# Optimization experiments

Hardware: AMD Instinct MI355X
Metric: run time of the kernel (lower is better)

Reference implementation:

```python
import jax, jax.numpy as jnp
import numpy as np

NEG_SLOPE = 0.2
EPS = 1e-16
HEADS1, OUT1 = 4, 32
HEADS2, OUT2 = 1, 32


def _gat_conv(x, W, a_src, a_dst, bias, src, dst, num_nodes, heads, out_c, concat):
    # x: [N, F_in], W: [F_in, heads*out_c], a_*: [heads, out_c]
    h = (x @ W).reshape(num_nodes, heads, out_c)            # [N, H, C]
    alpha_src = (h * a_src).sum(-1)                          # [N, H]
    alpha_dst = (h * a_dst).sum(-1)                          # [N, H]
    e = jax.nn.leaky_relu(alpha_src[src] + alpha_dst[dst], NEG_SLOPE)  # [E, H]
    # softmax over incoming edges of each destination node (PyG softmax)
    m = jax.ops.segment_max(e, dst, num_segments=num_nodes)
    ex = jnp.exp(e - m[dst])
    s = jax.ops.segment_sum(ex, dst, num_segments=num_nodes)
    alpha = ex / (s[dst] + EPS)                              # [E, H]
    out = jax.ops.segment_sum(h[src] * alpha[:, :, None], dst,
                              num_segments=num_nodes)        # [N, H, C]
    out = out.reshape(num_nodes, heads * out_c) if concat else out.mean(axis=1)
    return out + bias


def setup_inputs() -> dict:
    key = jax.random.key(0)
    ks = jax.random.split(key, 10)
    N, E, F_IN = 50000, 1600000, 128
    sc = 0.1
    return {
        "x": jax.random.normal(ks[0], (N, F_IN), jnp.float32),
        "edge_index": jax.random.randint(ks[1], (2, E), 0, N, jnp.int32),
        "W1": jax.random.normal(ks[2], (F_IN, HEADS1 * OUT1), jnp.float32) * sc,
        "a_src1": jax.random.normal(ks[3], (HEADS1, OUT1), jnp.float32) * sc,
        "a_dst1": jax.random.normal(ks[4], (HEADS1, OUT1), jnp.float32) * sc,
        "b1": jax.random.normal(ks[5], (HEADS1 * OUT1,), jnp.float32) * sc,
        "W2": jax.random.normal(ks[6], (HEADS1 * OUT1, HEADS2 * OUT2), jnp.float32) * sc,
        "a_src2": jax.random.normal(ks[7], (HEADS2, OUT2), jnp.float32) * sc,
        "a_dst2": jax.random.normal(ks[8], (HEADS2, OUT2), jnp.float32) * sc,
        "b2": jax.random.normal(ks[9], (OUT2,), jnp.float32) * sc,
    }


def reference(x, edge_index, W1, a_src1, a_dst1, b1, W2, a_src2, a_dst2, b2):
    N = x.shape[0]
    # PyG GATConv default add_self_loops=True
    loops = jnp.arange(N, dtype=edge_index.dtype)
    src = jnp.concatenate([edge_index[0], loops])
    dst = jnp.concatenate([edge_index[1], loops])
    h = _gat_conv(x, W1, a_src1, a_dst1, b1, src, dst, N, HEADS1, OUT1, True)
    h = jax.nn.elu(h)
    return _gat_conv(h, W2, a_src2, a_dst2, b2, src, dst, N, HEADS2, OUT2, False)
```

## Files before the change

### kernel.cpp

```cpp
#include <hip/hip_runtime.h>
#include <math.h>

#define NEG_SLOPE 0.2f
#define EPSV 1e-16f
#define NPART 16

typedef _Float16 half4 __attribute__((ext_vector_type(4)));
typedef _Float16 half8 __attribute__((ext_vector_type(8)));


__global__ void k_hist_rank(const int* __restrict__ ei, int E, int ET, int N,
                            int* __restrict__ degp, int* __restrict__ rank){
    int i = blockIdx.x * 256 + threadIdx.x;
    if (i < ET){
        int d = (i < E) ? ei[E + i] : (i - E);
        int p = blockIdx.x & (NPART - 1);
        rank[i] = atomicAdd(&degp[p * N + d], 1);
    }
}

__global__ void k_scan_blk(const int* __restrict__ degp, int N,
                           int* __restrict__ rowptr, int* __restrict__ bsum){
    int b = blockIdx.x, t = threadIdx.x;
    int base = b * 1024 + t * 4;
    int v[4];
    #pragma unroll
    for (int j = 0; j < 4; j++){
        int n = base + j, s = 0;
        if (n < N){
            #pragma unroll
            for (int p = 0; p < NPART; p++) s += degp[p * N + n];
        }
        v[j] = s;
    }
    int s = v[0] + v[1] + v[2] + v[3];
    int lane = t & 63, wid = t >> 6;
    int x = s;
    #pragma unroll
    for (int off = 1; off < 64; off <<= 1){
        int y = __shfl_up(x, off, 64);
        if (lane >= off) x += y;
    }
    __shared__ int ws[4];
    if (lane == 63) ws[wid] = x;
    __syncthreads();
    int woff = 0;
    for (int w = 0; w < wid; w++) woff += ws[w];
    int run = woff + x - s;
    #pragma unroll
    for (int j = 0; j < 4; j++){
        if (base + j < N) rowptr[base + j] = run;
        run += v[j];
    }
    if (t == 255) bsum[b] = woff + x;
}

__global__ void k_finalize(const int* __restrict__ bsum, const int* __restrict__ degp,
                           int N, int ET,
                           int* __restrict__ rowptr, int* __restrict__ poff){
    int b = blockIdx.x, t = threadIdx.x;
    int n = b * 256 + t;
    int chunk = (b * 256) >> 10;
    int off = 0;
    for (int c = 0; c < chunk; c++) off += bsum[c];
    if (n < N){
        int r = rowptr[n] + off;
        rowptr[n] = r;
        int run = r;
        #pragma unroll
        for (int p = 0; p < NPART; p++){
            poff[p * N + n] = run;
            run += degp[p * N + n];
        }
    }
    if (n == 0) rowptr[N] = ET;
}

__launch_bounds__(256)
__global__ void k_scatter2(const int* __restrict__ ei, int E, int ET, int N,
                           const int* __restrict__ poff, const int* __restrict__ rank,
                           int* __restrict__ csr_src){
    int i = blockIdx.x * 256 + threadIdx.x;
    if (i >= ET) return;
    int s, d;
    if (i < E){ s = ei[i]; d = ei[E + i]; } else { s = i - E; d = s; }
    int p = blockIdx.x & (NPART - 1);
    csr_src[poff[p * N + d] + rank[i]] = s;
}


__launch_bounds__(256)
__global__ void k_gemm1(const float* __restrict__ x, const float* __restrict__ W1,
                        const float* __restrict__ a_src, const float* __restrict__ a_dst,
                        _Float16* __restrict__ h1h, float* __restrict__ asrc1,
                        float* __restrict__ adst1, int N){
    __shared__ float Wl[128 * 128];
    __shared__ float xl[32 * 128];
    int t = threadIdx.x;
    int cg = t & 31, ns = t >> 5;
    for (int idx = t; idx < 4096; idx += 256)
        *(float4*)&Wl[idx * 4] = *(const float4*)&W1[idx * 4];
    int n0 = blockIdx.x * 32;
    for (int idx = t; idx < 1024; idx += 256){
        int row = idx >> 5, k4 = idx & 31;
        float4 v = {0.f, 0.f, 0.f, 0.f};
        if (n0 + row < N) v = *(const float4*)&x[(size_t)(n0 + row) * 128 + k4 * 4];
        *(float4*)&xl[row * 128 + k4 * 4] = v;
    }
    __syncthreads();
    float4 acc0 = {0,0,0,0}, acc1 = {0,0,0,0}, acc2 = {0,0,0,0}, acc3 = {0,0,0,0};
    #pragma unroll 2
    for (int k = 0; k < 128; k += 4){
        float4 xv0 = *(float4*)&xl[(ns     ) * 128 + k];
        float4 xv1 = *(float4*)&xl[(ns +  8) * 128 + k];
        float4 xv2 = *(float4*)&xl[(ns + 16) * 128 + k];
        float4 xv3 = *(float4*)&xl[(ns + 24) * 128 + k];
        #pragma unroll
        for (int kk = 0; kk < 4; kk++){
            float4 w = *(float4*)&Wl[(k + kk) * 128 + cg * 4];
            float x0 = ((float*)&xv0)[kk];
            float x1 = ((float*)&xv1)[kk];
            float x2v= ((float*)&xv2)[kk];
            float x3 = ((float*)&xv3)[kk];
            acc0.x = fmaf(x0, w.x, acc0.x); acc0.y = fmaf(x0, w.y, acc0.y);
            acc0.z = fmaf(x0, w.z, acc0.z); acc0.w = fmaf(x0, w.w, acc0.w);
            acc1.x = fmaf(x1, w.x, acc1.x); acc1.y = fmaf(x1, w.y, acc1.y);
            acc1.z = fmaf(x1, w.z, acc1.z); acc1.w = fmaf(x1, w.w, acc1.w);
            acc2.x = fmaf(x2v, w.x, acc2.x); acc2.y = fmaf(x2v, w.y, acc2.y);
            acc2.z = fmaf(x2v, w.z, acc2.z); acc2.w = fmaf(x2v, w.w, acc2.w);
            acc3.x = fmaf(x3, w.x, acc3.x); acc3.y = fmaf(x3, w.y, acc3.y);
            acc3.z = fmaf(x3, w.z, acc3.z); acc3.w = fmaf(x3, w.w, acc3.w);
        }
    }
    float4 a4s = *(const float4*)&a_src[cg * 4];
    float4 a4d = *(const float4*)&a_dst[cg * 4];
    float4 accs[4] = {acc0, acc1, acc2, acc3};
    #pragma unroll
    for (int j = 0; j < 4; j++){
        int n = n0 + ns + 8 * j;
        if (n >= N) continue;
        float4 a = accs[j];
        half4 hv;
        hv.x = (_Float16)a.x; hv.y = (_Float16)a.y;
        hv.z = (_Float16)a.z; hv.w = (_Float16)a.w;
        *(half4*)&h1h[((size_t)n << 7) + (cg << 2)] = hv;
        float vs = a.x * a4s.x + a.y * a4s.y + a.z * a4s.z + a.w * a4s.w;
        float vd = a.x * a4d.x + a.y * a4d.y + a.z * a4d.z + a.w * a4d.w;
        #pragma unroll
        for (int m = 1; m <= 4; m <<= 1){
            vs += __shfl_xor(vs, m, 64);
            vd += __shfl_xor(vd, m, 64);
        }
        if ((cg & 7) == 0){
            int head = cg >> 3;
            asrc1[n * 4 + head] = vs;
            adst1[n * 4 + head] = vd;
        }
    }
}


__launch_bounds__(256)
__global__ void k_agg1(const int* __restrict__ rowptr, const int* __restrict__ csr_src,
                       const float* __restrict__ asrc1, const float* __restrict__ adst1,
                       const _Float16* __restrict__ h1h,
                       const float* __restrict__ b1, float* __restrict__ x2){
    int t = threadIdx.x;
    int n = blockIdx.x * 4 + (t >> 6);
    int lane = t & 63, g = lane >> 4, l = lane & 15, head = l >> 2;
    int start = rowptr[n], end = rowptr[n + 1];
    float adn = adst1[(n << 2) + head];
    const char* hb = (const char*)h1h;
    const char* ab = (const char*)asrc1;
    int hoff = l << 4;
    int aoff = head << 2;
    float rA[8] = {0,0,0,0,0,0,0,0}, rB[8] = {0,0,0,0,0,0,0,0};
    float sA = 0.f, sB = 0.f;
    int i = start + g;
    for (; i + 4 < end; i += 8){
        int s0 = csr_src[i];
        int s1 = csr_src[i + 4];
        float e0 = *(const float*)(ab + (s0 << 4) + aoff) + adn;
        float e1 = *(const float*)(ab + (s1 << 4) + aoff) + adn;
        e0 = fmaxf(e0, NEG_SLOPE * e0);
        e1 = fmaxf(e1, NEG_SLOPE * e1);
        float w0 = __expf(e0);
        float w1 = __expf(e1);
        half8 h0 = *(const half8*)(hb + (s0 << 8) + hoff);
        half8 h1v = *(const half8*)(hb + (s1 << 8) + hoff);
        sA += w0; sB += w1;
        #pragma unroll
        for (int j = 0; j < 8; j++){
            rA[j] = fmaf(w0, (float)h0[j], rA[j]);
            rB[j] = fmaf(w1, (float)h1v[j], rB[j]);
        }
    }
    if (i < end){
        int s0 = csr_src[i];
        float e0 = *(const float*)(ab + (s0 << 4) + aoff) + adn;
        e0 = fmaxf(e0, NEG_SLOPE * e0);
        float w0 = __expf(e0);
        half8 h0 = *(const half8*)(hb + (s0 << 8) + hoff);
        sA += w0;
        #pragma unroll
        for (int j = 0; j < 8; j++) rA[j] = fmaf(w0, (float)h0[j], rA[j]);
    }
    float r[9];
    #pragma unroll
    for (int j = 0; j < 8; j++) r[j] = rA[j] + rB[j];
    r[8] = sA + sB;
    #pragma unroll
    for (int m = 16; m <= 32; m <<= 1)
        #pragma unroll
        for (int j = 0; j < 9; j++) r[j] += __shfl_xor(r[j], m, 64);
    if (g == 0){
        float inv = 1.f / (r[8] + EPSV);
        float o[8];
        #pragma unroll
        for (int j = 0; j < 8; j++){
            float v = r[j] * inv + b1[l * 8 + j];
            o[j] = (v > 0.f) ? v : expm1f(v);
        }
        float4 o0 = {o[0], o[1], o[2], o[3]};
        float4 o1 = {o[4], o[5], o[6], o[7]};
        *(float4*)&x2[((size_t)n << 7) + (l << 3)]     = o0;
        *(float4*)&x2[((size_t)n << 7) + (l << 3) + 4] = o1;
    }
}


__launch_bounds__(256)
__global__ void k_gemm2(const float* __restrict__ x2, const float* __restrict__ W2,
                        const float* __restrict__ a_src, const float* __restrict__ a_dst,
                        _Float16* __restrict__ h2h, float* __restrict__ asrc2,
                        float* __restrict__ adst2, int N){
    __shared__ float Wl[128 * 32];
    __shared__ float xl[128 * 128];
    int t = threadIdx.x;
    int cg = t & 7, ns = t >> 3;
    for (int idx = t; idx < 1024; idx += 256)
        *(float4*)&Wl[idx * 4] = *(const float4*)&W2[idx * 4];
    int n0 = blockIdx.x * 128;
    for (int idx = t; idx < 4096; idx += 256){
        int row = idx >> 5, k4 = idx & 31;
        float4 v = {0.f, 0.f, 0.f, 0.f};
        if (n0 + row < N) v = *(const float4*)&x2[(size_t)(n0 + row) * 128 + k4 * 4];
        *(float4*)&xl[row * 128 + k4 * 4] = v;
    }
    __syncthreads();
    float4 acc0 = {0,0,0,0}, acc1 = {0,0,0,0}, acc2 = {0,0,0,0}, acc3 = {0,0,0,0};
    #pragma unroll 2
    for (int k = 0; k < 128; k += 4){
        float4 xv0 = *(float4*)&xl[(ns      ) * 128 + k];
        float4 xv1 = *(float4*)&xl[(ns +  32) * 128 + k];
        float4 xv2 = *(float4*)&xl[(ns +  64) * 128 + k];
        float4 xv3 = *(float4*)&xl[(ns +  96) * 128 + k];
        #pragma unroll
        for (int kk = 0; kk < 4; kk++){
            float4 w = *(float4*)&Wl[(k + kk) * 32 + cg * 4];
            float x0 = ((float*)&xv0)[kk];
            float x1 = ((float*)&xv1)[kk];
            float x2v= ((float*)&xv2)[kk];
            float x3 = ((float*)&xv3)[kk];
            acc0.x = fmaf(x0, w.x, acc0.x); acc0.y = fmaf(x0, w.y, acc0.y);
            acc0.z = fmaf(x0, w.z, acc0.z); acc0.w = fmaf(x0, w.w, acc0.w);
            acc1.x = fmaf(x1, w.x, acc1.x); acc1.y = fmaf(x1, w.y, acc1.y);
            acc1.z = fmaf(x1, w.z, acc1.z); acc1.w = fmaf(x1, w.w, acc1.w);
            acc2.x = fmaf(x2v, w.x, acc2.x); acc2.y = fmaf(x2v, w.y, acc2.y);
            acc2.z = fmaf(x2v, w.z, acc2.z); acc2.w = fmaf(x2v, w.w, acc2.w);
            acc3.x = fmaf(x3, w.x, acc3.x); acc3.y = fmaf(x3, w.y, acc3.y);
            acc3.z = fmaf(x3, w.z, acc3.z); acc3.w = fmaf(x3, w.w, acc3.w);
        }
    }
    float4 a4s = *(const float4*)&a_src[cg * 4];
    float4 a4d = *(const float4*)&a_dst[cg * 4];
    float4 accs[4] = {acc0, acc1, acc2, acc3};
    #pragma unroll
    for (int j = 0; j < 4; j++){
        int n = n0 + ns + 32 * j;
        if (n >= N) continue;
        float4 a = accs[j];
        half4 hv;
        hv.x = (_Float16)a.x; hv.y = (_Float16)a.y;
        hv.z = (_Float16)a.z; hv.w = (_Float16)a.w;
        *(half4*)&h2h[((size_t)n << 5) + (cg << 2)] = hv;
        float vs = a.x * a4s.x + a.y * a4s.y + a.z * a4s.z + a.w * a4s.w;
        float vd = a.x * a4d.x + a.y * a4d.y + a.z * a4d.z + a.w * a4d.w;
        #pragma unroll
        for (int m = 1; m <= 4; m <<= 1){
            vs += __shfl_xor(vs, m, 64);
            vd += __shfl_xor(vd, m, 64);
        }
        if (cg == 0){ asrc2[n] = vs; adst2[n] = vd; }
    }
}


__launch_bounds__(256)
__global__ void k_agg2(const int* __restrict__ rowptr, const int* __restrict__ csr_src,
                       const float* __restrict__ asrc2, const float* __restrict__ adst2,
                       const _Float16* __restrict__ h2h,
                       const float* __restrict__ b2, float* __restrict__ out){
    int t = threadIdx.x;
    int n = blockIdx.x * 4 + (t >> 6);
    int lane = t & 63, g = lane >> 3, l = lane & 7;
    int start = rowptr[n], end = rowptr[n + 1];
    float adn = adst2[n];
    const char* hb = (const char*)h2h;
    const char* ab = (const char*)asrc2;
    int hoff = l << 3;
    float4 aA = {0,0,0,0}, aB = {0,0,0,0};
    float sA = 0.f, sB = 0.f;
    int i = start + g;
    for (; i + 8 < end; i += 16){
        int s0 = csr_src[i];
        int s1 = csr_src[i + 8];
        float e0 = *(const float*)(ab + (s0 << 2)) + adn;
        float e1 = *(const float*)(ab + (s1 << 2)) + adn;
        e0 = fmaxf(e0, NEG_SLOPE * e0);
        e1 = fmaxf(e1, NEG_SLOPE * e1);
        float w0 = __expf(e0);
        float w1 = __expf(e1);
        half4 h0 = *(const half4*)(hb + (s0 << 6) + hoff);
        half4 h1v = *(const half4*)(hb + (s1 << 6) + hoff);
        sA += w0; sB += w1;
        aA.x = fmaf(w0, (float)h0.x, aA.x); aA.y = fmaf(w0, (float)h0.y, aA.y);
        aA.z = fmaf(w0, (float)h0.z, aA.z); aA.w = fmaf(w0, (float)h0.w, aA.w);
        aB.x = fmaf(w1, (float)h1v.x, aB.x); aB.y = fmaf(w1, (float)h1v.y, aB.y);
        aB.z = fmaf(w1, (float)h1v.z, aB.z); aB.w = fmaf(w1, (float)h1v.w, aB.w);
    }
    if (i < end){
        int s0 = csr_src[i];
        float e0 = *(const float*)(ab + (s0 << 2)) + adn;
        e0 = fmaxf(e0, NEG_SLOPE * e0);
        float w0 = __expf(e0);
        half4 h0 = *(const half4*)(hb + (s0 << 6) + hoff);
        sA += w0;
        aA.x = fmaf(w0, (float)h0.x, aA.x); aA.y = fmaf(w0, (float)h0.y, aA.y);
        aA.z = fmaf(w0, (float)h0.z, aA.z); aA.w = fmaf(w0, (float)h0.w, aA.w);
    }
    float4 acc = {aA.x + aB.x, aA.y + aB.y, aA.z + aB.z, aA.w + aB.w};
    float ssum = sA + sB;
    #pragma unroll
    for (int m = 8; m <= 32; m <<= 1){
        acc.x += __shfl_xor(acc.x, m, 64);
        acc.y += __shfl_xor(acc.y, m, 64);
        acc.z += __shfl_xor(acc.z, m, 64);
        acc.w += __shfl_xor(acc.w, m, 64);
        ssum  += __shfl_xor(ssum,  m, 64);
    }
    if (g == 0){
        float inv = 1.f / (ssum + EPSV);
        const float4 b4 = *(const float4*)&b2[l * 4];
        float4 o;
        o.x = acc.x * inv + b4.x; o.y = acc.y * inv + b4.y;
        o.z = acc.z * inv + b4.z; o.w = acc.w * inv + b4.w;
        *(float4*)&out[((size_t)n << 5) + l * 4] = o;
    }
}


extern "C" void kernel_launch(void* const* d_in, const int* in_sizes, int n_in,
                              void* d_out, int out_size, void* d_ws, size_t ws_size,
                              hipStream_t stream){
    const float* x      = (const float*)d_in[0];
    const int*   ei     = (const int*)  d_in[1];
    const float* W1     = (const float*)d_in[2];
    const float* a_src1 = (const float*)d_in[3];
    const float* a_dst1 = (const float*)d_in[4];
    const float* b1     = (const float*)d_in[5];
    const float* W2     = (const float*)d_in[6];
    const float* a_src2 = (const float*)d_in[7];
    const float* a_dst2 = (const float*)d_in[8];
    const float* b2     = (const float*)d_in[9];
    float* out = (float*)d_out;

    int N  = in_sizes[0] / 128;
    int E  = in_sizes[1] / 2;
    int ET = E + N;
    int nScanBlk = (N + 1023) / 1024;
    int G  = (ET + 255) / 256;

    char* ws = (char*)d_ws;
    size_t off = 0;
    auto alloc = [&](size_t bytes) -> char* {
        char* p = ws + off;
        off += (bytes + 255) & ~(size_t)255;
        return p;
    };
    int*      degp    = (int*)     alloc((size_t)NPART * N * 4);
    int*      rowptr  = (int*)     alloc((size_t)(N + 1) * 4);
    int*      bsum    = (int*)     alloc((size_t)nScanBlk * 4);
    int*      rank    = (int*)     alloc((size_t)ET * 4);
    int*      poff    = (int*)     alloc((size_t)NPART * N * 4);
    int*      csr_src = (int*)     alloc((size_t)ET * 4);
    _Float16* h1h     = (_Float16*)alloc((size_t)N * 128 * 2);
    float*    x2      = (float*)   alloc((size_t)N * 128 * 4);
    float*    asrc1   = (float*)   alloc((size_t)N * 4 * 4);
    float*    adst1   = (float*)   alloc((size_t)N * 4 * 4);
    _Float16* h2h     = (_Float16*)alloc((size_t)N * 32 * 2);
    float*    asrc2   = (float*)   alloc((size_t)N * 4);
    float*    adst2   = (float*)   alloc((size_t)N * 4);

    hipMemsetAsync(degp, 0, (size_t)NPART * N * 4, stream);
    hipLaunchKernelGGL(k_hist_rank, dim3(G), dim3(256), 0, stream, ei, E, ET, N, degp, rank);
    hipLaunchKernelGGL(k_scan_blk,  dim3(nScanBlk), dim3(256), 0, stream, degp, N, rowptr, bsum);
    hipLaunchKernelGGL(k_finalize,  dim3((N + 255) / 256), dim3(256), 0, stream, bsum, degp, N, ET, rowptr, poff);
    hipLaunchKernelGGL(k_scatter2,  dim3(G), dim3(256), 0, stream, ei, E, ET, N, poff, rank, csr_src);
    hipLaunchKernelGGL(k_gemm1,     dim3((N + 31) / 32), dim3(256), 0, stream, x, W1, a_src1, a_dst1, h1h, asrc1, adst1, N);
    hipLaunchKernelGGL(k_agg1,      dim3(N / 4), dim3(256), 0, stream, rowptr, csr_src, asrc1, adst1, h1h, b1, x2);
    hipLaunchKernelGGL(k_gemm2,     dim3((N + 127) / 128), dim3(256), 0, stream, x2, W2, a_src2, a_dst2, h2h, asrc2, adst2, N);
    hipLaunchKernelGGL(k_agg2,      dim3(N / 4), dim3(256), 0, stream, rowptr, csr_src, asrc2, adst2, h2h, b2, out);
}
```

Measured before the change: 337.5 us.

## Fuse degree histogram into gemm1 launch and shrink rank to 16-bit

```diff
diff --git a/kernel.cpp b/kernel.cpp
--- a/kernel.cpp
+++ b/kernel.cpp
@@ -8,16 +8,6 @@
 typedef _Float16 half4 __attribute__((ext_vector_type(4)));
 typedef _Float16 half8 __attribute__((ext_vector_type(8)));
 
-
-__global__ void k_hist_rank(const int* __restrict__ ei, int E, int ET, int N,
-                            int* __restrict__ degp, int* __restrict__ rank){
-    int i = blockIdx.x * 256 + threadIdx.x;
-    if (i < ET){
-        int d = (i < E) ? ei[E + i] : (i - E);
-        int p = blockIdx.x & (NPART - 1);
-        rank[i] = atomicAdd(&degp[p * N + d], 1);
-    }
-}
 
 __global__ void k_scan_blk(const int* __restrict__ degp, int N,
                            int* __restrict__ rowptr, int* __restrict__ bsum){
@@ -78,25 +68,37 @@
 
 __launch_bounds__(256)
 __global__ void k_scatter2(const int* __restrict__ ei, int E, int ET, int N,
-                           const int* __restrict__ poff, const int* __restrict__ rank,
+                           const int* __restrict__ poff,
+                           const unsigned short* __restrict__ rank,
                            int* __restrict__ csr_src){
     int i = blockIdx.x * 256 + threadIdx.x;
     if (i >= ET) return;
     int s, d;
     if (i < E){ s = ei[i]; d = ei[E + i]; } else { s = i - E; d = s; }
-    int p = blockIdx.x & (NPART - 1);
-    csr_src[poff[p * N + d] + rank[i]] = s;
+    int p = (i >> 8) & (NPART - 1);
+    csr_src[poff[p * N + d] + (int)rank[i]] = s;
 }
 
 
 __launch_bounds__(256)
-__global__ void k_gemm1(const float* __restrict__ x, const float* __restrict__ W1,
-                        const float* __restrict__ a_src, const float* __restrict__ a_dst,
-                        _Float16* __restrict__ h1h, float* __restrict__ asrc1,
-                        float* __restrict__ adst1, int N){
+__global__ void k_gemm1_hist(const float* __restrict__ x, const float* __restrict__ W1,
+                             const float* __restrict__ a_src, const float* __restrict__ a_dst,
+                             _Float16* __restrict__ h1h, float* __restrict__ asrc1,
+                             float* __restrict__ adst1, int N, int nGemmBlk,
+                             const int* __restrict__ ei, int E, int ET,
+                             int* __restrict__ degp, unsigned short* __restrict__ rank){
     __shared__ float Wl[128 * 128];
     __shared__ float xl[32 * 128];
     int t = threadIdx.x;
+    if ((int)blockIdx.x >= nGemmBlk){
+        int i = (blockIdx.x - nGemmBlk) * 256 + t;
+        if (i < ET){
+            int d = (i < E) ? ei[E + i] : (i - E);
+            int p = (i >> 8) & (NPART - 1);
+            rank[i] = (unsigned short)atomicAdd(&degp[p * N + d], 1);
+        }
+        return;
+    }
     int cg = t & 31, ns = t >> 5;
     for (int idx = t; idx < 4096; idx += 256)
         *(float4*)&Wl[idx * 4] = *(const float4*)&W1[idx * 4];
@@ -380,6 +382,7 @@
     int ET = E + N;
     int nScanBlk = (N + 1023) / 1024;
     int G  = (ET + 255) / 256;
+    int nGemmBlk = (N + 31) / 32;
 
     char* ws = (char*)d_ws;
     size_t off = 0;
@@ -388,26 +391,27 @@
         off += (bytes + 255) & ~(size_t)255;
         return p;
     };
-    int*      degp    = (int*)     alloc((size_t)NPART * N * 4);
-    int*      rowptr  = (int*)     alloc((size_t)(N + 1) * 4);
-    int*      bsum    = (int*)     alloc((size_t)nScanBlk * 4);
-    int*      rank    = (int*)     alloc((size_t)ET * 4);
-    int*      poff    = (int*)     alloc((size_t)NPART * N * 4);
-    int*      csr_src = (int*)     alloc((size_t)ET * 4);
-    _Float16* h1h     = (_Float16*)alloc((size_t)N * 128 * 2);
-    float*    x2      = (float*)   alloc((size_t)N * 128 * 4);
-    float*    asrc1   = (float*)   alloc((size_t)N * 4 * 4);
-    float*    adst1   = (float*)   alloc((size_t)N * 4 * 4);
-    _Float16* h2h     = (_Float16*)alloc((size_t)N * 32 * 2);
-    float*    asrc2   = (float*)   alloc((size_t)N * 4);
-    float*    adst2   = (float*)   alloc((size_t)N * 4);
+    int*            degp    = (int*)           alloc((size_t)NPART * N * 4);
+    int*            rowptr  = (int*)           alloc((size_t)(N + 1) * 4);
+    int*            bsum    = (int*)           alloc((size_t)nScanBlk * 4);
+    unsigned short* rank    = (unsigned short*)alloc((size_t)ET * 2);
+    int*            poff    = (int*)           alloc((size_t)NPART * N * 4);
+    int*            csr_src = (int*)           alloc((size_t)ET * 4);
+    _Float16*       h1h     = (_Float16*)      alloc((size_t)N * 128 * 2);
+    float*          x2      = (float*)         alloc((size_t)N * 128 * 4);
+    float*          asrc1   = (float*)         alloc((size_t)N * 4 * 4);
+    float*          adst1   = (float*)         alloc((size_t)N * 4 * 4);
+    _Float16*       h2h     = (_Float16*)      alloc((size_t)N * 32 * 2);
+    float*          asrc2   = (float*)         alloc((size_t)N * 4);
+    float*          adst2   = (float*)         alloc((size_t)N * 4);
 
     hipMemsetAsync(degp, 0, (size_t)NPART * N * 4, stream);
-    hipLaunchKernelGGL(k_hist_rank, dim3(G), dim3(256), 0, stream, ei, E, ET, N, degp, rank);
+    hipLaunchKernelGGL(k_gemm1_hist, dim3(nGemmBlk + G), dim3(256), 0, stream,
+                       x, W1, a_src1, a_dst1, h1h, asrc1, adst1, N, nGemmBlk,
+                       ei, E, ET, degp, rank);
     hipLaunchKernelGGL(k_scan_blk,  dim3(nScanBlk), dim3(256), 0, stream, degp, N, rowptr, bsum);
     hipLaunchKernelGGL(k_finalize,  dim3((N + 255) / 256), dim3(256), 0, stream, bsum, degp, N, ET, rowptr, poff);
     hipLaunchKernelGGL(k_scatter2,  dim3(G), dim3(256), 0, stream, ei, E, ET, N, poff, rank, csr_src);
-    hipLaunchKernelGGL(k_gemm1,     dim3((N + 31) / 32), dim3(256), 0, stream, x, W1, a_src1, a_dst1, h1h, asrc1, adst1, N);
     hipLaunchKernelGGL(k_agg1,      dim3(N / 4), dim3(256), 0, stream, rowptr, csr_src, asrc1, adst1, h1h, b1, x2);
     hipLaunchKernelGGL(k_gemm2,     dim3((N + 127) / 128), dim3(256), 0, stream, x2, W2, a_src2, a_dst2, h2h, asrc2, adst2, N);
     hipLaunchKernelGGL(k_agg2,      dim3(N / 4), dim3(256), 0, stream, rowptr, csr_src, asrc2, adst2, h2h, b2, out);
```

Measured after the change: 324.7 us. 1.04x faster.
